# Performance work log

Hardware: AMD Instinct MI355X
Metric: run time of the kernel (lower is better)

Reference implementation:

```python
import jax, jax.numpy as jnp
import numpy as np

B, L, D, H, NB = 64, 30, 512, 8, 6
AS, MT = 18, 4096
T = 3 * L
HD = D // H
EPS = 1e-3  # keras LayerNormalization default epsilon
CONV_FEAT = 7 * 7 * 64  # 84 ->(8,s4) 20 ->(4,s2) 9 ->(3,s1) 7


def setup_inputs() -> dict:
    key = jax.random.key(0)
    ks = iter(jax.random.split(key, 64))
    r = lambda *s: jax.random.normal(next(ks), s, jnp.float32) * 0.02
    inp = {
        'rtgs': jax.random.normal(next(ks), (B, L, 1), jnp.float32),
        'states': jax.random.uniform(next(ks), (B, L, 84, 84, 4), jnp.float32) * 255.0,
        'actions': jax.random.randint(next(ks), (B, L, 1), 0, AS),
        'timesteps': jax.random.randint(next(ks), (B, 1, 1), 0, MT + 1),
        # rtg embedding
        'W_rtg': r(1, D), 'b_rtg': r(D),
        # state conv stem (HWIO)
        'conv1_w': r(8, 8, 4, 32), 'conv1_b': r(32),
        'conv2_w': r(4, 4, 32, 64), 'conv2_b': r(64),
        'conv3_w': r(3, 3, 64, 64), 'conv3_b': r(64),
        'dense_s_w': r(CONV_FEAT, D), 'dense_s_b': r(D),
        # action embedding table
        'emb_a': r(AS, D),
        # positional embeddings
        'abs_pos': r(1, MT + 1, D), 'rel_pos': r(1, T + 1, D),
        # decoder blocks (stacked over NB)
        'ln1_g': 1.0 + r(NB, D), 'ln1_b': r(NB, D),
        'Wk': r(NB, D, D), 'bk': r(NB, D),
        'Wq': r(NB, D, D), 'bq': r(NB, D),
        'Wv': r(NB, D, D), 'bv': r(NB, D),
        'ln2_g': 1.0 + r(NB, D), 'ln2_b': r(NB, D),
        'W1': r(NB, D, 4 * D), 'b1': r(NB, 4 * D),
        'W2': r(NB, 4 * D, D), 'b2': r(NB, D),
        # final norm + head (no bias)
        'lnf_g': 1.0 + r(D), 'lnf_b': r(D),
        'W_head': r(D, AS),
    }
    return inp


def _conv(x, w, b, stride):
    y = jax.lax.conv_general_dilated(x, w, (stride, stride), 'VALID',
                                     dimension_numbers=('NHWC', 'HWIO', 'NHWC'))
    return jax.nn.relu(y + b)


def _layernorm(x, g, b):
    m = x.mean(-1, keepdims=True)
    v = ((x - m) ** 2).mean(-1, keepdims=True)
    return (x - m) / jnp.sqrt(v + EPS) * g + b


def _attn(x, Wk, bk, Wq, bq, Wv, bv):
    Bx, Tx, C = x.shape
    split = lambda z: z.reshape(Bx, Tx, H, HD).transpose(0, 2, 1, 3)  # (B,H,T,hd)
    k, q, v = split(x @ Wk + bk), split(x @ Wq + bq), split(x @ Wv + bv)
    # NOTE: faithful to source: scores = K @ Q^T (not Q @ K^T)
    s = jnp.einsum('bhid,bhjd->bhij', k, q) / jnp.sqrt(jnp.float32(HD))
    mask = jnp.tril(jnp.ones((Tx, Tx), bool))
    s = jnp.where(mask, s, -jnp.inf)
    w = jax.nn.softmax(s, axis=-1)
    o = jnp.einsum('bhij,bhjd->bhid', w, v)
    return o.transpose(0, 2, 1, 3).reshape(Bx, Tx, C)


def reference(rtgs, states, actions, timesteps, W_rtg, b_rtg,
              conv1_w, conv1_b, conv2_w, conv2_b, conv3_w, conv3_b,
              dense_s_w, dense_s_b, emb_a, abs_pos, rel_pos,
              ln1_g, ln1_b, Wk, bk, Wq, bq, Wv, bv,
              ln2_g, ln2_b, W1, b1, W2, b2, lnf_g, lnf_b, W_head):
    # embeddings
    rtg_e = jnp.tanh(rtgs @ W_rtg + b_rtg)                       # (B,L,D)
    s = states.reshape(B * L, 84, 84, 4) / 255.0
    s = _conv(s, conv1_w, conv1_b, 4)
    s = _conv(s, conv2_w, conv2_b, 2)
    s = _conv(s, conv3_w, conv3_b, 1)
    st_e = jnp.tanh(s.reshape(B, L, -1) @ dense_s_w + dense_s_b)  # (B,L,D)
    a_e = jnp.tanh(emb_a[actions[..., 0]])                        # (B,L,D)
    # positional: abs gathered at start timestep + relative
    abs_e = abs_pos[0][timesteps[:, 0, 0]][:, None, :]            # (B,1,D)
    pos = rel_pos[:, :T, :] + abs_e                               # (B,3L,D)
    # interleave (rtg, state, action) per timestep
    tokens = jnp.stack([rtg_e, st_e, a_e], axis=2).reshape(B, T, D)
    x = tokens + pos
    for i in range(NB):
        h = _layernorm(x, ln1_g[i], ln1_b[i])
        x = x + _attn(h, Wk[i], bk[i], Wq[i], bq[i], Wv[i], bv[i])
        h = _layernorm(x, ln2_g[i], ln2_b[i])
        x = x + jax.nn.gelu(h @ W1[i] + b1[i], approximate=False) @ W2[i] + b2[i]
    x = _layernorm(x, lnf_g, lnf_b)
    logits = x @ W_head                                           # (B,3L,AS)
    return logits[:, 1::3, :]                                     # state positions -> (B,L,AS)
```

## Files before the change

kernel.cpp:

```cpp
#include <hip/hip_runtime.h>
#include <hip/hip_bf16.h>

typedef __attribute__((ext_vector_type(8))) __bf16 bf16x8;
typedef __attribute__((ext_vector_type(4))) float f32x4;

#define ACT_NONE 0
#define ACT_RELU 1
#define ACT_GELU 2
#define ACT_TANH 3
#define OUT_F32 0
#define OUT_BF16 1
#define OUT_ADD 2

__device__ __forceinline__ void gll16(const void* g, void* l) {
  __builtin_amdgcn_global_load_lds(
      reinterpret_cast<const __attribute__((address_space(1))) unsigned int*>(
          reinterpret_cast<unsigned long long>(g)),
      reinterpret_cast<__attribute__((address_space(3))) unsigned int*>(
          reinterpret_cast<unsigned long long>(l)),
      16, 0, 0);
}

template<int MODE, int K>
__device__ __forceinline__ size_t a_rowbase(int m) {
  if constexpr (MODE == 0) {
    return (size_t)m * K;
  } else if constexpr (MODE == 1) {
    int img = m / 400; int p = m - img * 400; int oy = p / 20; int ox = p - oy * 20;
    return (size_t)img * 28224 + oy * 1344 + ox * 16;
  } else if constexpr (MODE == 2) {
    int img = m / 81; int p = m - img * 81; int oy = p / 9; int ox = p - oy * 9;
    return (size_t)img * 12800 + oy * 1280 + ox * 64;
  } else {
    int img = m / 49; int p = m - img * 49; int oy = p / 7; int ox = p - oy * 7;
    return (size_t)img * 5184 + oy * 576 + ox * 64;
  }
}
template<int MODE>
__device__ __forceinline__ int f_koff(int kb) {
  if constexpr (MODE == 0) return kb;
  else if constexpr (MODE == 2) return (kb >> 7) * 640 + ((kb >> 5) & 3) * 32;
  else return kb + (kb / 192) * 384;
}

__device__ __forceinline__ bf16x8 ld8f(const float* f) {
  float4 a = *(const float4*)f;
  float4 b = *(const float4*)(f + 4);
  bf16x8 r;
  r[0] = (__bf16)a.x; r[1] = (__bf16)a.y; r[2] = (__bf16)a.z; r[3] = (__bf16)a.w;
  r[4] = (__bf16)b.x; r[5] = (__bf16)b.y; r[6] = (__bf16)b.z; r[7] = (__bf16)b.w;
  return r;
}

__device__ __forceinline__ float act_apply(float v, int ACT) {
  if (ACT == ACT_RELU) return fmaxf(v, 0.f);
  if (ACT == ACT_GELU) return 0.5f * v * (1.f + erff(v * 0.70710678118f));
  if (ACT == ACT_TANH) return tanhf(v);
  return v;
}

template<int MODE, int TM, int TN, int WM, int WN, int K, int ACT, int OUTM, int LDC>
__global__ __launch_bounds__(256) void gemm_k(const __bf16* __restrict__ A,
                                              const __bf16* __restrict__ BT,
                                              const float* __restrict__ bias,
                                              void* __restrict__ C) {
  constexpr int SM = TM / WM, SN = TN / WN;
  constexpr int AM = SM / 16, AN = SN / 16;
  constexpr int TA = TM / 64, TB = TN / 64;
  __shared__ __align__(16) __bf16 As[TM * 32];
  __shared__ __align__(16) __bf16 Bs[TN * 32];
  const int tid = threadIdx.x;
  const int wave = tid >> 6, lane = tid & 63;
  const int quad = lane >> 4, l16 = lane & 15;
  const int wr = wave % WM, wc = wave / WM;
  const int m0 = blockIdx.x * TM, n0 = blockIdx.y * TN;
  const int lrow = lane >> 2, lkc = lane & 3;

  const __bf16* ga[TA];
  const __bf16* gb[TB];
#pragma unroll
  for (int t = 0; t < TA; ++t)
    ga[t] = A + a_rowbase<MODE, K>(m0 + (wave + 4 * t) * 16 + lrow) + lkc * 8;
#pragma unroll
  for (int t = 0; t < TB; ++t)
    gb[t] = BT + (size_t)(n0 + (wave + 4 * t) * 16 + lrow) * K + lkc * 8;

  f32x4 acc[AM][AN] = {};
  for (int kt = 0; kt < K / 32; ++kt) {
    const int kb = kt * 32;
    const int fa = f_koff<MODE>(kb);
    __syncthreads();
#pragma unroll
    for (int t = 0; t < TA; ++t)
      gll16(ga[t] + fa, &As[(wave + 4 * t) * 16 * 32]);
#pragma unroll
    for (int t = 0; t < TB; ++t)
      gll16(gb[t] + kb, &Bs[(wave + 4 * t) * 16 * 32]);
    __syncthreads();
    bf16x8 af[AM], bf[AN];
#pragma unroll
    for (int mt = 0; mt < AM; ++mt)
      af[mt] = *(const bf16x8*)&As[(wr * SM + mt * 16 + l16) * 32 + quad * 8];
#pragma unroll
    for (int nt = 0; nt < AN; ++nt)
      bf[nt] = *(const bf16x8*)&Bs[(wc * SN + nt * 16 + l16) * 32 + quad * 8];
#pragma unroll
    for (int mt = 0; mt < AM; ++mt)
#pragma unroll
      for (int nt = 0; nt < AN; ++nt)
        acc[mt][nt] = __builtin_amdgcn_mfma_f32_16x16x32_bf16(af[mt], bf[nt], acc[mt][nt], 0, 0, 0);
  }

#pragma unroll
  for (int nt = 0; nt < AN; ++nt) {
    const int col = n0 + wc * SN + nt * 16 + l16;
    const float bvl = bias[col];
#pragma unroll
    for (int mt = 0; mt < AM; ++mt) {
#pragma unroll
      for (int r = 0; r < 4; ++r) {
        const int row = m0 + wr * SM + mt * 16 + quad * 4 + r;
        float v = act_apply(acc[mt][nt][r] + bvl, ACT);
        const size_t off = (size_t)row * LDC + col;
        if constexpr (OUTM == OUT_F32) ((float*)C)[off] = v;
        else if constexpr (OUTM == OUT_BF16) ((__bf16*)C)[off] = (__bf16)v;
        else ((float*)C)[off] += v;
      }
    }
  }
}

__global__ __launch_bounds__(256) void conv1_k(const float* __restrict__ A,
                                               const __bf16* __restrict__ BT,
                                               const float* __restrict__ bias,
                                               __bf16* __restrict__ C) {
  __shared__ __align__(16) __bf16 As[128 * 32];
  __shared__ __align__(16) __bf16 Bs[32 * 32];
  const int tid = threadIdx.x;
  const int wave = tid >> 6, lane = tid & 63;
  const int quad = lane >> 4, l16 = lane & 15;
  const int m0 = blockIdx.x * 128;
  const int lrow = lane >> 2, lkc = lane & 3;
  const int r0 = tid >> 2, k0o = (tid & 3) * 8;
  const int r1 = r0 + 64;
  const size_t ar0 = a_rowbase<1, 256>(m0 + r0);
  const size_t ar1 = a_rowbase<1, 256>(m0 + r1);
  const __bf16* gB = BT + (size_t)(wave * 16 + lrow) * 256 + lkc * 8;

  f32x4 acc[2][2] = {};
  bf16x8 a0 = ld8f(A + ar0 + k0o);
  bf16x8 a1 = ld8f(A + ar1 + k0o);
  for (int kt = 0; kt < 8; ++kt) {
    const int kb = kt * 32;
    __syncthreads();
    if (wave < 2) gll16(gB + kb, &Bs[wave * 16 * 32]);
    *(bf16x8*)&As[r0 * 32 + k0o] = a0;
    *(bf16x8*)&As[r1 * 32 + k0o] = a1;
    __syncthreads();
    if (kt < 7) {
      const int fa = (kt + 1) * 336;
      a0 = ld8f(A + ar0 + fa + k0o);
      a1 = ld8f(A + ar1 + fa + k0o);
    }
    bf16x8 af[2], bf[2];
#pragma unroll
    for (int mt = 0; mt < 2; ++mt)
      af[mt] = *(const bf16x8*)&As[(wave * 32 + mt * 16 + l16) * 32 + quad * 8];
#pragma unroll
    for (int nt = 0; nt < 2; ++nt)
      bf[nt] = *(const bf16x8*)&Bs[(nt * 16 + l16) * 32 + quad * 8];
#pragma unroll
    for (int mt = 0; mt < 2; ++mt)
#pragma unroll
      for (int nt = 0; nt < 2; ++nt)
        acc[mt][nt] = __builtin_amdgcn_mfma_f32_16x16x32_bf16(af[mt], bf[nt], acc[mt][nt], 0, 0, 0);
  }
#pragma unroll
  for (int nt = 0; nt < 2; ++nt) {
    const int col = nt * 16 + l16;
    const float bvl = bias[col];
#pragma unroll
    for (int mt = 0; mt < 2; ++mt) {
#pragma unroll
      for (int r = 0; r < 4; ++r) {
        const int row = m0 + wave * 32 + mt * 16 + quad * 4 + r;
        C[(size_t)row * 32 + col] = (__bf16)fmaxf(acc[mt][nt][r] + bvl, 0.f);
      }
    }
  }
}

template<typename TO>
__global__ void transpose_pad(const float* __restrict__ src, TO* __restrict__ dst,
                              int R, int C, int Cpad, long long sz, long long dz, float scale) {
  src += blockIdx.z * sz; dst += blockIdx.z * dz;
  __shared__ float t[32][33];
  const int tx = threadIdx.x, ty = threadIdx.y;
  const int r0 = blockIdx.x * 32, c0 = blockIdx.y * 32;
  for (int i = ty; i < 32; i += 8) {
    int r = r0 + i, c = c0 + tx;
    t[i][tx] = (r < R && c < C) ? src[(size_t)r * C + c] : 0.f;
  }
  __syncthreads();
  for (int i = ty; i < 32; i += 8) {
    int c = c0 + i, r = r0 + tx;
    if (c < Cpad && r < R)
      dst[(size_t)c * R + r] = (c < C) ? (TO)(t[tx][i] * scale) : (TO)0.f;
  }
}

__global__ void biascat_k(const float* bk, const float* bq, const float* bv, float* dst) {
  const int i = blockIdx.x;
  for (int d = threadIdx.x; d < 512; d += 256) {
    dst[i * 1536 + d] = bk[i * 512 + d];
    dst[i * 1536 + 512 + d] = bq[i * 512 + d];
    dst[i * 1536 + 1024 + d] = bv[i * 512 + d];
  }
}

__global__ void embed_k(const float* __restrict__ rtgs, const int* __restrict__ actions,
                        const int* __restrict__ timesteps, const float* __restrict__ W_rtg,
                        const float* __restrict__ b_rtg, const float* __restrict__ emb_a,
                        const float* __restrict__ abs_pos, const float* __restrict__ rel_pos,
                        const float* __restrict__ ste, float* __restrict__ x) {
  const int idx = blockIdx.x * 256 + threadIdx.x;
  const int d = idx & 511; const int rb = idx >> 9;
  const int b = rb / 90, t = rb - b * 90;
  const int l = t / 3, r = t - l * 3;
  const float pos = rel_pos[t * 512 + d] + abs_pos[(size_t)timesteps[b] * 512 + d];
  float tok;
  if (r == 0) tok = tanhf(rtgs[b * 30 + l] * W_rtg[d] + b_rtg[d]);
  else if (r == 1) tok = ste[(size_t)(b * 30 + l) * 512 + d];
  else tok = tanhf(emb_a[actions[b * 30 + l] * 512 + d]);
  x[idx] = tok + pos;
}

__global__ __launch_bounds__(256) void ln_k(const float* __restrict__ x, const float* __restrict__ g,
                                            const float* __restrict__ bb, __bf16* __restrict__ h) {
  const int row = blockIdx.x * 4 + (threadIdx.x >> 6);
  const int lane = threadIdx.x & 63;
  const float* xr = x + (size_t)row * 512;
  float4 a = *(const float4*)&xr[lane * 8];
  float4 c = *(const float4*)&xr[lane * 8 + 4];
  float vv[8] = {a.x, a.y, a.z, a.w, c.x, c.y, c.z, c.w};
  float s = 0.f, q = 0.f;
#pragma unroll
  for (int j = 0; j < 8; ++j) { s += vv[j]; q += vv[j] * vv[j]; }
  for (int o = 32; o; o >>= 1) { s += __shfl_xor(s, o); q += __shfl_xor(q, o); }
  const float mean = s * (1.f / 512.f);
  const float var = q * (1.f / 512.f) - mean * mean;
  const float rstd = rsqrtf(var + 1e-3f);
  float4 g1 = *(const float4*)&g[lane * 8];
  float4 g2 = *(const float4*)&g[lane * 8 + 4];
  float4 b1 = *(const float4*)&bb[lane * 8];
  float4 b2 = *(const float4*)&bb[lane * 8 + 4];
  float gg[8] = {g1.x, g1.y, g1.z, g1.w, g2.x, g2.y, g2.z, g2.w};
  float bbv[8] = {b1.x, b1.y, b1.z, b1.w, b2.x, b2.y, b2.z, b2.w};
  bf16x8 ov;
#pragma unroll
  for (int j = 0; j < 8; ++j)
    ov[j] = (__bf16)((vv[j] - mean) * rstd * gg[j] + bbv[j]);
  *(bf16x8*)&h[(size_t)row * 512 + lane * 8] = ov;
}

__global__ __launch_bounds__(256) void attn_k(const __bf16* __restrict__ qkv, float* __restrict__ x) {
  __shared__ __align__(16) char smem[64512];
  __bf16* kS = (__bf16*)smem;
  __bf16* qS = (__bf16*)(smem + 13824);
  __bf16* wS = (__bf16*)smem;
  float* sS = (float*)(smem + 27648);
  __bf16* vT = (__bf16*)(smem + 27648);

  const int tid = threadIdx.x;
  const int b = blockIdx.x >> 3, h = blockIdx.x & 7;
  const int wave = tid >> 6, lane = tid & 63, quad = lane >> 4, l16 = lane & 15;
  const size_t rowbase = (size_t)b * 90 * 1536 + h * 64;

  for (int c = tid; c < 768; c += 256) {
    const int t = c >> 3, d8 = (c & 7) * 8;
    bf16x8 kv, qv;
#pragma unroll
    for (int j = 0; j < 8; ++j) { kv[j] = (__bf16)0.f; qv[j] = (__bf16)0.f; }
    if (t < 90) {
      const __bf16* src = qkv + rowbase + (size_t)t * 1536 + d8;
      kv = *(const bf16x8*)src;
      qv = *(const bf16x8*)(src + 512);
    }
    *(bf16x8*)&kS[t * 72 + d8] = kv;
    *(bf16x8*)&qS[t * 72 + d8] = qv;
  }
  __syncthreads();

  for (int tt = wave; tt < 36; tt += 4) {
    const int it = tt / 6, jt = tt - it * 6;
    f32x4 acc = {0.f, 0.f, 0.f, 0.f};
#pragma unroll
    for (int ks = 0; ks < 2; ++ks) {
      bf16x8 af = *(const bf16x8*)&kS[(it * 16 + l16) * 72 + ks * 32 + quad * 8];
      bf16x8 bq = *(const bf16x8*)&qS[(jt * 16 + l16) * 72 + ks * 32 + quad * 8];
      acc = __builtin_amdgcn_mfma_f32_16x16x32_bf16(af, bq, acc, 0, 0, 0);
    }
    const int col = jt * 16 + l16;
#pragma unroll
    for (int r = 0; r < 4; ++r) {
      const int row = it * 16 + quad * 4 + r;
      sS[row * 96 + col] = (col <= row && col < 90) ? acc[r] * 0.125f : -1e30f;
    }
  }
  __syncthreads();

  for (int row = wave; row < 96; row += 4) {
    const float e0 = sS[row * 96 + lane];
    const float e1 = (lane < 32) ? sS[row * 96 + 64 + lane] : -1e30f;
    float m = fmaxf(e0, e1);
    for (int o = 32; o; o >>= 1) m = fmaxf(m, __shfl_xor(m, o));
    const float p0 = __expf(e0 - m);
    const float p1 = (lane < 32) ? __expf(e1 - m) : 0.f;
    float s = p0 + p1;
    for (int o = 32; o; o >>= 1) s += __shfl_xor(s, o);
    const float inv = 1.f / s;
    wS[row * 104 + lane] = (__bf16)(p0 * inv);
    if (lane < 32) wS[row * 104 + 64 + lane] = (__bf16)(p1 * inv);
  }
  __syncthreads();

  for (int c = tid; c < 768; c += 256) {
    const int t = c >> 3, d8 = (c & 7) * 8;
    bf16x8 vv;
#pragma unroll
    for (int j = 0; j < 8; ++j) vv[j] = (__bf16)0.f;
    if (t < 90) vv = *(const bf16x8*)(qkv + rowbase + (size_t)t * 1536 + 1024 + d8);
#pragma unroll
    for (int j = 0; j < 8; ++j) vT[(d8 + j) * 104 + t] = vv[j];
  }
  __syncthreads();

  for (int tt = wave; tt < 24; tt += 4) {
    const int it = tt >> 2, dt = tt & 3;
    f32x4 acc = {0.f, 0.f, 0.f, 0.f};
#pragma unroll
    for (int ks = 0; ks < 3; ++ks) {
      bf16x8 aw = *(const bf16x8*)&wS[(it * 16 + l16) * 104 + ks * 32 + quad * 8];
      bf16x8 bv = *(const bf16x8*)&vT[(dt * 16 + l16) * 104 + ks * 32 + quad * 8];
      acc = __builtin_amdgcn_mfma_f32_16x16x32_bf16(aw, bv, acc, 0, 0, 0);
    }
    const int d = dt * 16 + l16;
#pragma unroll
    for (int r = 0; r < 4; ++r) {
      const int i = it * 16 + quad * 4 + r;
      if (i < 90) {
        float* p = x + (size_t)(b * 90 + i) * 512 + h * 64 + d;
        *p += acc[r];
      }
    }
  }
}

__global__ __launch_bounds__(64) void head_k(const float* __restrict__ x, const float* __restrict__ g,
                                             const float* __restrict__ bb, const float* __restrict__ whT,
                                             float* __restrict__ out) {
  const int m = blockIdx.x;
  const int b = m / 30, l = m - b * 30;
  const float* xr = x + (size_t)(b * 90 + 3 * l + 1) * 512;
  const int lane = threadIdx.x;
  float4 a = *(const float4*)&xr[lane * 8];
  float4 c = *(const float4*)&xr[lane * 8 + 4];
  float vv[8] = {a.x, a.y, a.z, a.w, c.x, c.y, c.z, c.w};
  float s = 0.f, q = 0.f;
#pragma unroll
  for (int j = 0; j < 8; ++j) { s += vv[j]; q += vv[j] * vv[j]; }
  for (int o = 32; o; o >>= 1) { s += __shfl_xor(s, o); q += __shfl_xor(q, o); }
  const float mean = s * (1.f / 512.f);
  const float var = q * (1.f / 512.f) - mean * mean;
  const float rstd = rsqrtf(var + 1e-3f);
  float4 g1 = *(const float4*)&g[lane * 8];
  float4 g2 = *(const float4*)&g[lane * 8 + 4];
  float4 b1 = *(const float4*)&bb[lane * 8];
  float4 b2 = *(const float4*)&bb[lane * 8 + 4];
  float gg[8] = {g1.x, g1.y, g1.z, g1.w, g2.x, g2.y, g2.z, g2.w};
  float bbv[8] = {b1.x, b1.y, b1.z, b1.w, b2.x, b2.y, b2.z, b2.w};
#pragma unroll
  for (int j = 0; j < 8; ++j)
    vv[j] = (vv[j] - mean) * rstd * gg[j] + bbv[j];
  for (int aa = 0; aa < 18; ++aa) {
    float4 w1v = *(const float4*)&whT[aa * 512 + lane * 8];
    float4 w2v = *(const float4*)&whT[aa * 512 + lane * 8 + 4];
    float ww[8] = {w1v.x, w1v.y, w1v.z, w1v.w, w2v.x, w2v.y, w2v.z, w2v.w};
    float d = 0.f;
#pragma unroll
    for (int j = 0; j < 8; ++j) d += vv[j] * ww[j];
    for (int o = 32; o; o >>= 1) d += __shfl_xor(d, o);
    if (lane == 0) out[m * 18 + aa] = d;
  }
}

extern "C" void kernel_launch(void* const* d_in, const int* in_sizes, int n_in,
                              void* d_out, int out_size, void* d_ws, size_t ws_size,
                              hipStream_t stream) {
  const float* rtgs = (const float*)d_in[0];
  const float* states = (const float*)d_in[1];
  const int* actions = (const int*)d_in[2];
  const int* timesteps = (const int*)d_in[3];
  const float* W_rtg = (const float*)d_in[4];
  const float* b_rtg = (const float*)d_in[5];
  const float* conv1_w = (const float*)d_in[6];
  const float* conv1_b = (const float*)d_in[7];
  const float* conv2_w = (const float*)d_in[8];
  const float* conv2_b = (const float*)d_in[9];
  const float* conv3_w = (const float*)d_in[10];
  const float* conv3_b = (const float*)d_in[11];
  const float* dense_s_w = (const float*)d_in[12];
  const float* dense_s_b = (const float*)d_in[13];
  const float* emb_a = (const float*)d_in[14];
  const float* abs_pos = (const float*)d_in[15];
  const float* rel_pos = (const float*)d_in[16];
  const float* ln1_g = (const float*)d_in[17];
  const float* ln1_b = (const float*)d_in[18];
  const float* Wk = (const float*)d_in[19];
  const float* bk = (const float*)d_in[20];
  const float* Wq = (const float*)d_in[21];
  const float* bq = (const float*)d_in[22];
  const float* Wv = (const float*)d_in[23];
  const float* bv = (const float*)d_in[24];
  const float* ln2_g = (const float*)d_in[25];
  const float* ln2_b = (const float*)d_in[26];
  const float* W1 = (const float*)d_in[27];
  const float* b1 = (const float*)d_in[28];
  const float* W2 = (const float*)d_in[29];
  const float* b2 = (const float*)d_in[30];
  const float* lnf_g = (const float*)d_in[31];
  const float* lnf_b = (const float*)d_in[32];
  const float* W_head = (const float*)d_in[33];
  float* out = (float*)d_out;

  char* W = (char*)d_ws;
  float* x = (float*)(W + 0);
  __bf16* h = (__bf16*)(W + 11796480);
  __bf16* qkvT = (__bf16*)(W + 17694720);
  __bf16* w1T = (__bf16*)(W + 27131904);
  __bf16* w2T = (__bf16*)(W + 39714816);
  __bf16* dswT = (__bf16*)(W + 52297728);
  __bf16* c1wT = (__bf16*)(W + 55508992);
  __bf16* c2wT = (__bf16*)(W + 55574528);
  __bf16* c3wT = (__bf16*)(W + 55705600);
  float* whT = (float*)(W + 55853056);
  float* bqkv = (float*)(W + 55889920);
  __bf16* c1out = (__bf16*)(W + 55926784);
  __bf16* c2out = (__bf16*)(W + 105078784);
  __bf16* c3out = (__bf16*)(W + 55926784);
  float* ste = (float*)(W + 67969024);
  __bf16* qkvb = (__bf16*)(W + 55926784);
  __bf16* mlph = (__bf16*)(W + 73621504);

  const dim3 tb(32, 8);
  transpose_pad<__bf16><<<dim3(8, 4, 1), tb, 0, stream>>>(conv1_w, c1wT, 256, 32, 128, 0, 0, 1.f / 255.f);
  transpose_pad<__bf16><<<dim3(16, 4, 1), tb, 0, stream>>>(conv2_w, c2wT, 512, 64, 128, 0, 0, 1.f);
  transpose_pad<__bf16><<<dim3(18, 4, 1), tb, 0, stream>>>(conv3_w, c3wT, 576, 64, 128, 0, 0, 1.f);
  transpose_pad<__bf16><<<dim3(98, 16, 1), tb, 0, stream>>>(dense_s_w, dswT, 3136, 512, 512, 0, 0, 1.f);
  transpose_pad<__bf16><<<dim3(16, 16, 6), tb, 0, stream>>>(Wk, qkvT, 512, 512, 512, 512 * 512, 1536 * 512, 1.f);
  transpose_pad<__bf16><<<dim3(16, 16, 6), tb, 0, stream>>>(Wq, qkvT + 512 * 512, 512, 512, 512, 512 * 512, 1536 * 512, 1.f);
  transpose_pad<__bf16><<<dim3(16, 16, 6), tb, 0, stream>>>(Wv, qkvT + 1024 * 512, 512, 512, 512, 512 * 512, 1536 * 512, 1.f);
  transpose_pad<__bf16><<<dim3(16, 64, 6), tb, 0, stream>>>(W1, w1T, 512, 2048, 2048, 512 * 2048, 2048 * 512, 1.f);
  transpose_pad<__bf16><<<dim3(64, 16, 6), tb, 0, stream>>>(W2, w2T, 2048, 512, 512, 2048 * 512, 512 * 2048, 1.f);
  transpose_pad<float><<<dim3(16, 1, 1), tb, 0, stream>>>(W_head, whT, 512, 18, 18, 0, 0, 1.f);
  biascat_k<<<6, 256, 0, stream>>>(bk, bq, bv, bqkv);

  conv1_k<<<6000, 256, 0, stream>>>(states, c1wT, conv1_b, c1out);
  gemm_k<2, 128, 64, 2, 2, 512, ACT_RELU, OUT_BF16, 64><<<dim3(1215, 1), 256, 0, stream>>>(c1out, c2wT, conv2_b, c2out);
  gemm_k<3, 128, 64, 2, 2, 576, ACT_RELU, OUT_BF16, 64><<<dim3(735, 1), 256, 0, stream>>>(c2out, c3wT, conv3_b, c3out);
  gemm_k<0, 64, 64, 2, 2, 3136, ACT_TANH, OUT_F32, 512><<<dim3(30, 8), 256, 0, stream>>>(c3out, dswT, dense_s_b, (void*)ste);

  embed_k<<<11520, 256, 0, stream>>>(rtgs, actions, timesteps, W_rtg, b_rtg, emb_a, abs_pos, rel_pos, ste, x);

  for (int i = 0; i < 6; ++i) {
    ln_k<<<1440, 256, 0, stream>>>(x, ln1_g + i * 512, ln1_b + i * 512, h);
    gemm_k<0, 128, 128, 2, 2, 512, ACT_NONE, OUT_BF16, 1536><<<dim3(45, 12), 256, 0, stream>>>(
        h, qkvT + (size_t)i * 1536 * 512, bqkv + i * 1536, qkvb);
    attn_k<<<512, 256, 0, stream>>>(qkvb, x);
    ln_k<<<1440, 256, 0, stream>>>(x, ln2_g + i * 512, ln2_b + i * 512, h);
    gemm_k<0, 128, 128, 2, 2, 512, ACT_GELU, OUT_BF16, 2048><<<dim3(45, 16), 256, 0, stream>>>(
        h, w1T + (size_t)i * 2048 * 512, b1 + i * 2048, mlph);
    gemm_k<0, 64, 128, 2, 2, 2048, ACT_NONE, OUT_ADD, 512><<<dim3(90, 4), 256, 0, stream>>>(
        mlph, w2T + (size_t)i * 2048 * 512, b2 + i * 512, x);
  }

  head_k<<<1920, 64, 0, stream>>>(x, lnf_g, lnf_b, whT, out);
}
```

Measured before the change: 1.386 ms.

## Add XCD block swizzle to conv GEMMs, prefetch V in attention, merge QKV transposes

Adds an XCD-aware block index remap so consecutive M tiles of conv1 and the conv2/conv3 GEMMs land on the same XCD, improving L2 locality of their overlapping input windows. The attention kernel issues the V global loads into registers early so their latency overlaps the score computation. The three QKV weight transposes become one launch. The W2 GEMM tile is shrunk to 64x64, doubling its grid to give more blocks for the CUs.

```diff
diff --git a/kernel.cpp b/kernel.cpp
--- a/kernel.cpp
+++ b/kernel.cpp
@@ -19,6 +19,11 @@
       reinterpret_cast<__attribute__((address_space(3))) unsigned int*>(
           reinterpret_cast<unsigned long long>(l)),
       16, 0, 0);
+}
+
+__device__ __forceinline__ int xcd_swz(int bid, int n) {
+  const int q = n >> 3, r = n & 7, x = bid & 7, o = bid >> 3;
+  return (x < r ? x * (q + 1) : r * (q + 1) + (x - r) * q) + o;
 }
 
 template<int MODE, int K>
@@ -59,7 +64,7 @@
   return v;
 }
 
-template<int MODE, int TM, int TN, int WM, int WN, int K, int ACT, int OUTM, int LDC>
+template<int MODE, int TM, int TN, int WM, int WN, int K, int ACT, int OUTM, int LDC, int SWZ>
 __global__ __launch_bounds__(256) void gemm_k(const __bf16* __restrict__ A,
                                               const __bf16* __restrict__ BT,
                                               const float* __restrict__ bias,
@@ -73,7 +78,8 @@
   const int wave = tid >> 6, lane = tid & 63;
   const int quad = lane >> 4, l16 = lane & 15;
   const int wr = wave % WM, wc = wave / WM;
-  const int m0 = blockIdx.x * TM, n0 = blockIdx.y * TN;
+  const int bm = SWZ ? xcd_swz(blockIdx.x, gridDim.x) : blockIdx.x;
+  const int m0 = bm * TM, n0 = blockIdx.y * TN;
   const int lrow = lane >> 2, lkc = lane & 3;
 
   const __bf16* ga[TA];
@@ -139,7 +145,7 @@
   const int tid = threadIdx.x;
   const int wave = tid >> 6, lane = tid & 63;
   const int quad = lane >> 4, l16 = lane & 15;
-  const int m0 = blockIdx.x * 128;
+  const int m0 = xcd_swz(blockIdx.x, gridDim.x) * 128;
   const int lrow = lane >> 2, lkc = lane & 3;
   const int r0 = tid >> 2, k0o = (tid & 3) * 8;
   const int r1 = r0 + 64;
@@ -207,6 +213,21 @@
     if (c < Cpad && r < R)
       dst[(size_t)c * R + r] = (c < C) ? (TO)(t[tx][i] * scale) : (TO)0.f;
   }
+}
+
+__global__ void transpose_qkv(const float* __restrict__ Wk_, const float* __restrict__ Wq_,
+                              const float* __restrict__ Wv_, __bf16* __restrict__ dst) {
+  const int z = blockIdx.z, which = z / 6, i = z - which * 6;
+  const float* src = (which == 0 ? Wk_ : which == 1 ? Wq_ : Wv_) + (size_t)i * 512 * 512;
+  __bf16* d = dst + (size_t)i * 1536 * 512 + (size_t)which * 512 * 512;
+  __shared__ float t[32][33];
+  const int tx = threadIdx.x, ty = threadIdx.y;
+  const int r0 = blockIdx.x * 32, c0 = blockIdx.y * 32;
+  for (int j = ty; j < 32; j += 8)
+    t[j][tx] = src[(size_t)(r0 + j) * 512 + c0 + tx];
+  __syncthreads();
+  for (int j = ty; j < 32; j += 8)
+    d[(size_t)(c0 + j) * 512 + r0 + tx] = (__bf16)t[tx][j];
 }
 
 __global__ void biascat_k(const float* bk, const float* bq, const float* bv, float* dst) {
@@ -276,6 +297,15 @@
   const int wave = tid >> 6, lane = tid & 63, quad = lane >> 4, l16 = lane & 15;
   const size_t rowbase = (size_t)b * 90 * 1536 + h * 64;
 
+  bf16x8 vreg[3];
+#pragma unroll
+  for (int it = 0; it < 3; ++it) {
+    const int c = tid + it * 256, t = c >> 3, d8 = (c & 7) * 8;
+#pragma unroll
+    for (int j = 0; j < 8; ++j) vreg[it][j] = (__bf16)0.f;
+    if (t < 90) vreg[it] = *(const bf16x8*)(qkv + rowbase + (size_t)t * 1536 + 1024 + d8);
+  }
+
   for (int c = tid; c < 768; c += 256) {
     const int t = c >> 3, d8 = (c & 7) * 8;
     bf16x8 kv, qv;
@@ -324,14 +354,11 @@
   }
   __syncthreads();
 
-  for (int c = tid; c < 768; c += 256) {
-    const int t = c >> 3, d8 = (c & 7) * 8;
-    bf16x8 vv;
-#pragma unroll
-    for (int j = 0; j < 8; ++j) vv[j] = (__bf16)0.f;
-    if (t < 90) vv = *(const bf16x8*)(qkv + rowbase + (size_t)t * 1536 + 1024 + d8);
-#pragma unroll
-    for (int j = 0; j < 8; ++j) vT[(d8 + j) * 104 + t] = vv[j];
+#pragma unroll
+  for (int it = 0; it < 3; ++it) {
+    const int c = tid + it * 256, t = c >> 3, d8 = (c & 7) * 8;
+#pragma unroll
+    for (int j = 0; j < 8; ++j) vT[(d8 + j) * 104 + t] = vreg[it][j];
   }
   __syncthreads();
 
@@ -457,30 +484,28 @@
   transpose_pad<__bf16><<<dim3(16, 4, 1), tb, 0, stream>>>(conv2_w, c2wT, 512, 64, 128, 0, 0, 1.f);
   transpose_pad<__bf16><<<dim3(18, 4, 1), tb, 0, stream>>>(conv3_w, c3wT, 576, 64, 128, 0, 0, 1.f);
   transpose_pad<__bf16><<<dim3(98, 16, 1), tb, 0, stream>>>(dense_s_w, dswT, 3136, 512, 512, 0, 0, 1.f);
-  transpose_pad<__bf16><<<dim3(16, 16, 6), tb, 0, stream>>>(Wk, qkvT, 512, 512, 512, 512 * 512, 1536 * 512, 1.f);
-  transpose_pad<__bf16><<<dim3(16, 16, 6), tb, 0, stream>>>(Wq, qkvT + 512 * 512, 512, 512, 512, 512 * 512, 1536 * 512, 1.f);
-  transpose_pad<__bf16><<<dim3(16, 16, 6), tb, 0, stream>>>(Wv, qkvT + 1024 * 512, 512, 512, 512, 512 * 512, 1536 * 512, 1.f);
+  transpose_qkv<<<dim3(16, 16, 18), tb, 0, stream>>>(Wk, Wq, Wv, qkvT);
   transpose_pad<__bf16><<<dim3(16, 64, 6), tb, 0, stream>>>(W1, w1T, 512, 2048, 2048, 512 * 2048, 2048 * 512, 1.f);
   transpose_pad<__bf16><<<dim3(64, 16, 6), tb, 0, stream>>>(W2, w2T, 2048, 512, 512, 2048 * 512, 512 * 2048, 1.f);
   transpose_pad<float><<<dim3(16, 1, 1), tb, 0, stream>>>(W_head, whT, 512, 18, 18, 0, 0, 1.f);
   biascat_k<<<6, 256, 0, stream>>>(bk, bq, bv, bqkv);
 
   conv1_k<<<6000, 256, 0, stream>>>(states, c1wT, conv1_b, c1out);
-  gemm_k<2, 128, 64, 2, 2, 512, ACT_RELU, OUT_BF16, 64><<<dim3(1215, 1), 256, 0, stream>>>(c1out, c2wT, conv2_b, c2out);
-  gemm_k<3, 128, 64, 2, 2, 576, ACT_RELU, OUT_BF16, 64><<<dim3(735, 1), 256, 0, stream>>>(c2out, c3wT, conv3_b, c3out);
-  gemm_k<0, 64, 64, 2, 2, 3136, ACT_TANH, OUT_F32, 512><<<dim3(30, 8), 256, 0, stream>>>(c3out, dswT, dense_s_b, (void*)ste);
+  gemm_k<2, 128, 64, 2, 2, 512, ACT_RELU, OUT_BF16, 64, 1><<<dim3(1215, 1), 256, 0, stream>>>(c1out, c2wT, conv2_b, c2out);
+  gemm_k<3, 128, 64, 2, 2, 576, ACT_RELU, OUT_BF16, 64, 1><<<dim3(735, 1), 256, 0, stream>>>(c2out, c3wT, conv3_b, c3out);
+  gemm_k<0, 64, 64, 2, 2, 3136, ACT_TANH, OUT_F32, 512, 0><<<dim3(30, 8), 256, 0, stream>>>(c3out, dswT, dense_s_b, (void*)ste);
 
   embed_k<<<11520, 256, 0, stream>>>(rtgs, actions, timesteps, W_rtg, b_rtg, emb_a, abs_pos, rel_pos, ste, x);
 
   for (int i = 0; i < 6; ++i) {
     ln_k<<<1440, 256, 0, stream>>>(x, ln1_g + i * 512, ln1_b + i * 512, h);
-    gemm_k<0, 128, 128, 2, 2, 512, ACT_NONE, OUT_BF16, 1536><<<dim3(45, 12), 256, 0, stream>>>(
+    gemm_k<0, 128, 128, 2, 2, 512, ACT_NONE, OUT_BF16, 1536, 0><<<dim3(45, 12), 256, 0, stream>>>(
         h, qkvT + (size_t)i * 1536 * 512, bqkv + i * 1536, qkvb);
     attn_k<<<512, 256, 0, stream>>>(qkvb, x);
     ln_k<<<1440, 256, 0, stream>>>(x, ln2_g + i * 512, ln2_b + i * 512, h);
-    gemm_k<0, 128, 128, 2, 2, 512, ACT_GELU, OUT_BF16, 2048><<<dim3(45, 16), 256, 0, stream>>>(
+    gemm_k<0, 128, 128, 2, 2, 512, ACT_GELU, OUT_BF16, 2048, 0><<<dim3(45, 16), 256, 0, stream>>>(
         h, w1T + (size_t)i * 2048 * 512, b1 + i * 2048, mlph);
-    gemm_k<0, 64, 128, 2, 2, 2048, ACT_NONE, OUT_ADD, 512><<<dim3(90, 4), 256, 0, stream>>>(
+    gemm_k<0, 64, 64, 2, 2, 2048, ACT_NONE, OUT_ADD, 512, 0><<<dim3(90, 8), 256, 0, stream>>>(
         mlph, w2T + (size_t)i * 2048 * 512, b2 + i * 512, x);
   }
 
```

Result: no change. 1.373 ms (-0.9%).
